# Kernel optimization log

Hardware: AMD Instinct MI355X
Metric: run time of the kernel (lower is better)

The kernel has to match this reference:

```python
import jax, jax.numpy as jnp
from jax import lax
import numpy as np


def _lstm_layer(x, Wih, Whh, bih, bhh):
    # x: [B,T,I]; Wih: [4H,I]; Whh: [4H,H]; gate order i,f,g,o (PyTorch).
    B = x.shape[0]
    H = Whh.shape[1]
    xg = jnp.einsum('bti,gi->btg', x, Wih) + bih + bhh  # [B,T,4H]

    def step(carry, xg_t):
        h, c = carry
        g = xg_t + h @ Whh.T  # [B,4H]
        i, f, gg, o = jnp.split(g, 4, axis=-1)
        i = jax.nn.sigmoid(i)
        f = jax.nn.sigmoid(f)
        gg = jnp.tanh(gg)
        o = jax.nn.sigmoid(o)
        c = f * c + i * gg
        h = o * jnp.tanh(c)
        return (h, c), h

    init = (jnp.zeros((B, H), x.dtype), jnp.zeros((B, H), x.dtype))
    _, hs = lax.scan(step, init, jnp.swapaxes(xg, 0, 1))  # hs: [T,B,H]
    return jnp.swapaxes(hs, 0, 1)  # [B,T,H]


def _uniform(key, shape, k):
    return jax.random.uniform(key, shape, jnp.float32, -k, k)


def setup_inputs() -> dict:
    key = jax.random.key(0)
    ks = jax.random.split(key, 20)
    B, T, D = 64, 512, 2048
    x = jax.random.normal(ks[0], (B, T, D), jnp.float32)
    inp = {'x': x}
    # PyTorch LSTM init: U(-1/sqrt(H), 1/sqrt(H))
    specs = [('1', 2048, 256), ('2', 256, 128), ('3', 128, 64)]
    i = 1
    for tag, I, H in specs:
        k = 1.0 / np.sqrt(H)
        inp['Wih' + tag] = _uniform(ks[i], (4 * H, I), k); i += 1
        inp['Whh' + tag] = _uniform(ks[i], (4 * H, H), k); i += 1
        inp['bih' + tag] = _uniform(ks[i], (4 * H,), k); i += 1
        inp['bhh' + tag] = _uniform(ks[i], (4 * H,), k); i += 1
    kd = 1.0 / np.sqrt(64)
    inp['Wd'] = _uniform(ks[13], (32, 64), kd)
    inp['bd'] = _uniform(ks[14], (32,), kd)
    kw = 1.0 / np.sqrt(2048)
    inp['Ww'] = _uniform(ks[15], (32, 2048), kw)
    inp['bw'] = _uniform(ks[16], (32,), kw)
    ko = 1.0 / np.sqrt(64)
    inp['Wo'] = _uniform(ks[17], (1, 64), ko)
    inp['bo'] = _uniform(ks[18], (1,), ko)
    return inp


def reference(x, Wih1, Whh1, bih1, bhh1, Wih2, Whh2, bih2, bhh2,
              Wih3, Whh3, bih3, bhh3, Wd, bd, Ww, bw, Wo, bo):
    out = _lstm_layer(x, Wih1, Whh1, bih1, bhh1)   # [B,T,256]
    out = _lstm_layer(out, Wih2, Whh2, bih2, bhh2)  # [B,T,128]
    out = _lstm_layer(out, Wih3, Whh3, bih3, bhh3)  # [B,T,64]
    deep = out[:, -1, :]                            # dropout is identity at eval
    deep = jax.nn.relu(deep @ Wd.T + bd)            # [B,32]
    wide = x[:, -1, :]
    wide = jax.nn.relu(wide @ Ww.T + bw)            # [B,32]
    comb = jnp.concatenate([deep, wide], axis=1)    # [B,64]
    return comb @ Wo.T + bo                         # [B,1]
```

## Files before the change

### kernel.cpp

```cpp
#include <hip/hip_runtime.h>

typedef _Float16 f16;
typedef _Float16 f16x2 __attribute__((ext_vector_type(2)));
typedef _Float16 f16x8 __attribute__((ext_vector_type(8)));
typedef float    f32x4 __attribute__((ext_vector_type(4)));

__device__ __forceinline__ f16x2 as_h2(unsigned int u) {
  union { unsigned int u; f16x2 h; } c; c.u = u; return c.h;
}
__device__ __forceinline__ unsigned int pack2(float x, float y) {
  union { f16x2 h; unsigned int u; } c; c.h = f16x2{(f16)x, (f16)y}; return c.u;
}
__device__ __forceinline__ float dot2f(unsigned int w, unsigned int h, float acc) {
#if __has_builtin(__builtin_amdgcn_fdot2)
  return __builtin_amdgcn_fdot2(as_h2(w), as_h2(h), acc, false);
#else
  f16x2 a = as_h2(w), b = as_h2(h);
  return acc + (float)a.x * (float)b.x + (float)a.y * (float)b.y;
#endif
}
__device__ __forceinline__ float sigmoidf_(float x) { return 1.f / (1.f + __expf(-x)); }
__device__ __forceinline__ float tanhf_(float x) { float e = __expf(2.f * x); return 1.f - 2.f / (e + 1.f); }

#define GLDS(gsrc, ldst) __builtin_amdgcn_global_load_lds( \
    (const __attribute__((address_space(1))) void*)(gsrc), \
    (__attribute__((address_space(3))) void*)(ldst), 16, 0, 0)

__global__ void cvt_f32_f16(const float* __restrict__ in, f16* __restrict__ out, long n) {
  long i = ((long)blockIdx.x * blockDim.x + threadIdx.x) * 8;
  long stride = (long)gridDim.x * blockDim.x * 8;
  for (; i < n; i += stride) {
    float4 a = *(const float4*)(in + i);
    float4 b = *(const float4*)(in + i + 4);
    f16x8 h = {(f16)a.x, (f16)a.y, (f16)a.z, (f16)a.w,
               (f16)b.x, (f16)b.y, (f16)b.z, (f16)b.w};
    *(f16x8*)(out + i) = h;
  }
}

template<int K>
__global__ __launch_bounds__(256) void gemm_bias(const f16* __restrict__ A,
                                                 const f16* __restrict__ W,
                                                 const float* __restrict__ bias1,
                                                 const float* __restrict__ bias2,
                                                 float* __restrict__ out, int N) {
  constexpr int BK = 32;
  __shared__ f16 As[2][128 * BK];
  __shared__ f16 Bs[2][128 * BK];
  const int tid = threadIdx.x;
  const int wid = tid >> 6, lane = tid & 63;
  const int m0 = blockIdx.x * 128, n0 = blockIdx.y * 128;
  const int wr = (wid >> 1) * 64, wc = (wid & 1) * 64;
  const int r = lane & 15, kg = lane >> 4;

  f32x4 acc[4][4];
  #pragma unroll
  for (int i = 0; i < 4; ++i)
    #pragma unroll
    for (int j = 0; j < 4; ++j) acc[i][j] = f32x4{0.f, 0.f, 0.f, 0.f};

  auto stage = [&](int buf, int k0) {
    #pragma unroll
    for (int i = 0; i < 2; ++i) {
      int c = tid + 256 * i;
      const f16* asrc = A + (long)(m0 + (c >> 2)) * K + k0 + (c & 3) * 8;
      GLDS(asrc, &As[buf][(64 * wid + 256 * i) * 8]);
      const f16* wsrc = W + (long)(n0 + (c >> 2)) * K + k0 + (c & 3) * 8;
      GLDS(wsrc, &Bs[buf][(64 * wid + 256 * i) * 8]);
    }
  };

  stage(0, 0);
  for (int kt = 0; kt < K / BK; ++kt) {
    __syncthreads();
    if (kt + 1 < K / BK) stage((kt + 1) & 1, (kt + 1) * BK);
    const f16* Ab = As[kt & 1];
    const f16* Bb = Bs[kt & 1];
    f16x8 af[4], bf[4];
    #pragma unroll
    for (int f = 0; f < 4; ++f) {
      af[f] = *(const f16x8*)&Ab[(wr + f * 16 + r) * BK + kg * 8];
      bf[f] = *(const f16x8*)&Bb[(wc + f * 16 + r) * BK + kg * 8];
    }
    #pragma unroll
    for (int mf = 0; mf < 4; ++mf)
      #pragma unroll
      for (int nf = 0; nf < 4; ++nf)
        acc[mf][nf] = __builtin_amdgcn_mfma_f32_16x16x32_f16(af[mf], bf[nf], acc[mf][nf], 0, 0, 0);
  }

  #pragma unroll
  for (int nf = 0; nf < 4; ++nf) {
    int n = n0 + wc + nf * 16 + r;
    float bsum = bias1[n] + bias2[n];
    #pragma unroll
    for (int mf = 0; mf < 4; ++mf) {
      #pragma unroll
      for (int q = 0; q < 4; ++q) {
        int m = m0 + wr + mf * 16 + kg * 4 + q;
        out[(long)m * N + n] = acc[mf][nf][q] + bsum;
      }
    }
  }
}

__global__ __launch_bounds__(512) void lstm_l1(const float* __restrict__ xg,
                                               const float* __restrict__ Whh,
                                               f16* __restrict__ hout) {
  __shared__ uint2 wtail[16][1024];
  __shared__ uint4 hbuf[32];
  __shared__ float gact[1024];
  const int b = blockIdx.x;
  const int t = threadIdx.x;
  const int g0 = t, g1 = t + 512;

  unsigned int w0[96], w1[96];
  #pragma unroll
  for (int p = 0; p < 96; ++p) {
    float2 f0 = *(const float2*)&Whh[g0 * 256 + 2 * p];
    float2 f1 = *(const float2*)&Whh[g1 * 256 + 2 * p];
    w0[p] = pack2(f0.x, f0.y);
    w1[p] = pack2(f1.x, f1.y);
  }
  #pragma unroll
  for (int u = 0; u < 16; ++u) {
    float4 f0 = *(const float4*)&Whh[g0 * 256 + 192 + 4 * u];
    wtail[u][g0] = make_uint2(pack2(f0.x, f0.y), pack2(f0.z, f0.w));
    float4 f1 = *(const float4*)&Whh[g1 * 256 + 192 + 4 * u];
    wtail[u][g1] = make_uint2(pack2(f1.x, f1.y), pack2(f1.z, f1.w));
  }
  if (t < 32) hbuf[t] = make_uint4(0, 0, 0, 0);
  float c = 0.f;
  __syncthreads();

  const bool g1_sig = (t >= 256);
  for (int ts = 0; ts < 512; ++ts) {
    const long base = ((long)b * 512 + ts);
    float a0 = xg[base * 1024 + g0];
    float a1 = xg[base * 1024 + g1];
    #pragma unroll
    for (int i = 0; i < 24; ++i) {
      uint4 hv = hbuf[i];
      a0 = dot2f(w0[4 * i + 0], hv.x, a0); a0 = dot2f(w0[4 * i + 1], hv.y, a0);
      a0 = dot2f(w0[4 * i + 2], hv.z, a0); a0 = dot2f(w0[4 * i + 3], hv.w, a0);
      a1 = dot2f(w1[4 * i + 0], hv.x, a1); a1 = dot2f(w1[4 * i + 1], hv.y, a1);
      a1 = dot2f(w1[4 * i + 2], hv.z, a1); a1 = dot2f(w1[4 * i + 3], hv.w, a1);
    }
    #pragma unroll
    for (int i = 0; i < 8; ++i) {
      uint4 hv = hbuf[24 + i];
      uint2 wa0 = wtail[2 * i][g0], wb0 = wtail[2 * i + 1][g0];
      uint2 wa1 = wtail[2 * i][g1], wb1 = wtail[2 * i + 1][g1];
      a0 = dot2f(wa0.x, hv.x, a0); a0 = dot2f(wa0.y, hv.y, a0);
      a0 = dot2f(wb0.x, hv.z, a0); a0 = dot2f(wb0.y, hv.w, a0);
      a1 = dot2f(wa1.x, hv.x, a1); a1 = dot2f(wa1.y, hv.y, a1);
      a1 = dot2f(wb1.x, hv.z, a1); a1 = dot2f(wb1.y, hv.w, a1);
    }
    gact[g0] = sigmoidf_(a0);
    gact[g1] = g1_sig ? sigmoidf_(a1) : tanhf_(a1);
    __syncthreads();
    if (t < 256) {
      float i_ = gact[t], f_ = gact[256 + t], gg = gact[512 + t], o_ = gact[768 + t];
      c = f_ * c + i_ * gg;
      float hn = o_ * tanhf_(c);
      reinterpret_cast<f16*>(hbuf)[t] = (f16)hn;
      hout[base * 256 + t] = (f16)hn;
    }
    __syncthreads();
  }
}

__global__ __launch_bounds__(512) void lstm_l2(const float* __restrict__ xg,
                                               const float* __restrict__ Whh,
                                               f16* __restrict__ hout) {
  __shared__ uint2 wlds[32][512];
  __shared__ uint4 hbuf[16];
  __shared__ float gact[512];
  const int b = blockIdx.x, t = threadIdx.x;
  #pragma unroll
  for (int u = 0; u < 32; ++u) {
    float4 f = *(const float4*)&Whh[t * 128 + 4 * u];
    wlds[u][t] = make_uint2(pack2(f.x, f.y), pack2(f.z, f.w));
  }
  if (t < 16) hbuf[t] = make_uint4(0, 0, 0, 0);
  float c = 0.f;
  __syncthreads();
  const int type = t >> 7;
  for (int ts = 0; ts < 512; ++ts) {
    const long base = ((long)b * 512 + ts);
    float a = xg[base * 512 + t];
    #pragma unroll
    for (int i = 0; i < 16; ++i) {
      uint4 hv = hbuf[i];
      uint2 wa = wlds[2 * i][t], wb = wlds[2 * i + 1][t];
      a = dot2f(wa.x, hv.x, a); a = dot2f(wa.y, hv.y, a);
      a = dot2f(wb.x, hv.z, a); a = dot2f(wb.y, hv.w, a);
    }
    gact[t] = (type == 2) ? tanhf_(a) : sigmoidf_(a);
    __syncthreads();
    if (t < 128) {
      float i_ = gact[t], f_ = gact[128 + t], gg = gact[256 + t], o_ = gact[384 + t];
      c = f_ * c + i_ * gg;
      float hn = o_ * tanhf_(c);
      reinterpret_cast<f16*>(hbuf)[t] = (f16)hn;
      hout[base * 128 + t] = (f16)hn;
    }
    __syncthreads();
  }
}

__global__ __launch_bounds__(256) void lstm_l3(const float* __restrict__ xg,
                                               const float* __restrict__ Whh,
                                               float* __restrict__ h3last) {
  __shared__ uint2 wlds[16][256];
  __shared__ uint4 hbuf[8];
  __shared__ float gact[256];
  const int b = blockIdx.x, t = threadIdx.x;
  #pragma unroll
  for (int u = 0; u < 16; ++u) {
    float4 f = *(const float4*)&Whh[t * 64 + 4 * u];
    wlds[u][t] = make_uint2(pack2(f.x, f.y), pack2(f.z, f.w));
  }
  if (t < 8) hbuf[t] = make_uint4(0, 0, 0, 0);
  float c = 0.f;
  __syncthreads();
  const int type = t >> 6;
  for (int ts = 0; ts < 512; ++ts) {
    float a = xg[((long)b * 512 + ts) * 256 + t];
    #pragma unroll
    for (int i = 0; i < 8; ++i) {
      uint4 hv = hbuf[i];
      uint2 wa = wlds[2 * i][t], wb = wlds[2 * i + 1][t];
      a = dot2f(wa.x, hv.x, a); a = dot2f(wa.y, hv.y, a);
      a = dot2f(wb.x, hv.z, a); a = dot2f(wb.y, hv.w, a);
    }
    gact[t] = (type == 2) ? tanhf_(a) : sigmoidf_(a);
    __syncthreads();
    if (t < 64) {
      float i_ = gact[t], f_ = gact[64 + t], gg = gact[128 + t], o_ = gact[192 + t];
      c = f_ * c + i_ * gg;
      float hn = o_ * tanhf_(c);
      reinterpret_cast<f16*>(hbuf)[t] = (f16)hn;
      if (ts == 511) h3last[b * 64 + t] = hn;
    }
    __syncthreads();
  }
}

__global__ __launch_bounds__(256) void head_kernel(const float* __restrict__ x,
                                                   const float* __restrict__ h3last,
                                                   const float* __restrict__ Wd, const float* __restrict__ bd,
                                                   const float* __restrict__ Ww, const float* __restrict__ bw,
                                                   const float* __restrict__ Wo, const float* __restrict__ bo,
                                                   float* __restrict__ outp) {
  __shared__ float part[256];
  __shared__ float comb[64];
  const int b = blockIdx.x, t = threadIdx.x;
  const int o = t & 31, seg = t >> 5;
  const float* xl = x + ((long)b * 512 + 511) * 2048;
  float s = 0.f;
  for (int k = seg * 256; k < seg * 256 + 256; ++k) s += xl[k] * Ww[o * 2048 + k];
  part[t] = s;
  __syncthreads();
  if (t < 32) {
    float w = 0.f;
    #pragma unroll
    for (int q = 0; q < 8; ++q) w += part[t + 32 * q];
    w += bw[t];
    comb[32 + t] = fmaxf(w, 0.f);
    float d = bd[t];
    for (int k = 0; k < 64; ++k) d += h3last[b * 64 + k] * Wd[t * 64 + k];
    comb[t] = fmaxf(d, 0.f);
  }
  __syncthreads();
  if (t == 0) {
    float r = bo[0];
    for (int j = 0; j < 64; ++j) r += comb[j] * Wo[j];
    outp[b] = r;
  }
}

static inline int cvt_blocks(long n) {
  long bl = (n / 8 + 255) / 256;
  return (int)(bl > 4096 ? 4096 : bl);
}

extern "C" void kernel_launch(void* const* d_in, const int* in_sizes, int n_in,
                              void* d_out, int out_size, void* d_ws, size_t ws_size,
                              hipStream_t stream) {
  const float* x    = (const float*)d_in[0];
  const float* Wih1 = (const float*)d_in[1];
  const float* Whh1 = (const float*)d_in[2];
  const float* bih1 = (const float*)d_in[3];
  const float* bhh1 = (const float*)d_in[4];
  const float* Wih2 = (const float*)d_in[5];
  const float* Whh2 = (const float*)d_in[6];
  const float* bih2 = (const float*)d_in[7];
  const float* bhh2 = (const float*)d_in[8];
  const float* Wih3 = (const float*)d_in[9];
  const float* Whh3 = (const float*)d_in[10];
  const float* bih3 = (const float*)d_in[11];
  const float* bhh3 = (const float*)d_in[12];
  const float* Wd   = (const float*)d_in[13];
  const float* bd   = (const float*)d_in[14];
  const float* Ww   = (const float*)d_in[15];
  const float* bw   = (const float*)d_in[16];
  const float* Wo   = (const float*)d_in[17];
  const float* bo   = (const float*)d_in[18];

  char* ws = (char*)d_ws;
  f16*   x_h   = (f16*)(ws + 0);
  float* xg1   = (float*)(ws + 134217728);
  f16*   h1    = (f16*)(ws + 268435456);
  f16*   wih1h = (f16*)(ws + 285212672);
  f16*   wih2h = (f16*)(ws + 289406976);
  f16*   wih3h = (f16*)(ws + 289669120);
  float* h3l   = (float*)(ws + 289734656);
  float* xg2   = (float*)(ws + 0);
  f16*   h2    = (f16*)(ws + 134217728);
  float* xg3   = (float*)(ws + 67108864);

  cvt_f32_f16<<<cvt_blocks(67108864), 256, 0, stream>>>(x, x_h, 67108864L);
  cvt_f32_f16<<<cvt_blocks(2097152), 256, 0, stream>>>(Wih1, wih1h, 2097152L);
  cvt_f32_f16<<<cvt_blocks(131072), 256, 0, stream>>>(Wih2, wih2h, 131072L);
  cvt_f32_f16<<<cvt_blocks(32768), 256, 0, stream>>>(Wih3, wih3h, 32768L);

  gemm_bias<2048><<<dim3(256, 8), 256, 0, stream>>>(x_h, wih1h, bih1, bhh1, xg1, 1024);
  lstm_l1<<<64, 512, 0, stream>>>(xg1, Whh1, h1);
  gemm_bias<256><<<dim3(256, 4), 256, 0, stream>>>(h1, wih2h, bih2, bhh2, xg2, 512);
  lstm_l2<<<64, 512, 0, stream>>>(xg2, Whh2, h2);
  gemm_bias<128><<<dim3(256, 2), 256, 0, stream>>>(h2, wih3h, bih3, bhh3, xg3, 256);
  lstm_l3<<<64, 256, 0, stream>>>(xg3, Whh3, h3l);
  head_kernel<<<64, 256, 0, stream>>>(x, h3l, Wd, bd, Ww, bw, Wo, bo, (float*)d_out);
}
```

Before: 2.724 ms.

## Prefetch next-step gate inputs, split dot accumulators, move small-layer weights to registers

In all three recurrent kernels, the next timestep's precomputed input-gate values are loaded during the current step, so global load latency leaves the serial critical path. The recurrent dot products now alternate between two accumulators, shortening the dependent fdot2 chain. Layers 2 and 3 keep their packed recurrent weights in registers instead of LDS, and layer 1 shifts a few weight columns from registers into LDS and adds a two-waves-per-SIMD launch-bounds hint. The cost is higher register pressure in layers 2 and 3, more LDS reads in layer 1, and possible spills if the compiler cannot meet the occupancy hint.

After: 2.308 ms. 15.3% less time.

```diff
diff --git a/kernel.cpp b/kernel.cpp
--- a/kernel.cpp
+++ b/kernel.cpp
@@ -104,29 +104,29 @@
   }
 }
 
-__global__ __launch_bounds__(512) void lstm_l1(const float* __restrict__ xg,
-                                               const float* __restrict__ Whh,
-                                               f16* __restrict__ hout) {
-  __shared__ uint2 wtail[16][1024];
+__global__ __launch_bounds__(512, 2) void lstm_l1(const float* __restrict__ xg,
+                                                  const float* __restrict__ Whh,
+                                                  f16* __restrict__ hout) {
+  __shared__ uint2 wtail[18][1024];
   __shared__ uint4 hbuf[32];
   __shared__ float gact[1024];
   const int b = blockIdx.x;
   const int t = threadIdx.x;
   const int g0 = t, g1 = t + 512;
 
-  unsigned int w0[96], w1[96];
-  #pragma unroll
-  for (int p = 0; p < 96; ++p) {
+  unsigned int w0[92], w1[92];
+  #pragma unroll
+  for (int p = 0; p < 92; ++p) {
     float2 f0 = *(const float2*)&Whh[g0 * 256 + 2 * p];
     float2 f1 = *(const float2*)&Whh[g1 * 256 + 2 * p];
     w0[p] = pack2(f0.x, f0.y);
     w1[p] = pack2(f1.x, f1.y);
   }
   #pragma unroll
-  for (int u = 0; u < 16; ++u) {
-    float4 f0 = *(const float4*)&Whh[g0 * 256 + 192 + 4 * u];
+  for (int u = 0; u < 18; ++u) {
+    float4 f0 = *(const float4*)&Whh[g0 * 256 + 184 + 4 * u];
     wtail[u][g0] = make_uint2(pack2(f0.x, f0.y), pack2(f0.z, f0.w));
-    float4 f1 = *(const float4*)&Whh[g1 * 256 + 192 + 4 * u];
+    float4 f1 = *(const float4*)&Whh[g1 * 256 + 184 + 4 * u];
     wtail[u][g1] = make_uint2(pack2(f1.x, f1.y), pack2(f1.z, f1.w));
   }
   if (t < 32) hbuf[t] = make_uint4(0, 0, 0, 0);
@@ -134,28 +134,48 @@
   __syncthreads();
 
   const bool g1_sig = (t >= 256);
+  const long rowbase = (long)b * 512;
+  float a0 = xg[rowbase * 1024 + g0];
+  float a1 = xg[rowbase * 1024 + g1];
   for (int ts = 0; ts < 512; ++ts) {
-    const long base = ((long)b * 512 + ts);
-    float a0 = xg[base * 1024 + g0];
-    float a1 = xg[base * 1024 + g1];
-    #pragma unroll
-    for (int i = 0; i < 24; ++i) {
+    const long base = rowbase + ts;
+    const long nb = rowbase + (ts < 511 ? ts + 1 : 511);
+    float a0n = xg[nb * 1024 + g0];
+    float a1n = xg[nb * 1024 + g1];
+    float s0 = 0.f, s1 = 0.f;
+    #pragma unroll
+    for (int i = 0; i < 23; ++i) {
       uint4 hv = hbuf[i];
-      a0 = dot2f(w0[4 * i + 0], hv.x, a0); a0 = dot2f(w0[4 * i + 1], hv.y, a0);
-      a0 = dot2f(w0[4 * i + 2], hv.z, a0); a0 = dot2f(w0[4 * i + 3], hv.w, a0);
-      a1 = dot2f(w1[4 * i + 0], hv.x, a1); a1 = dot2f(w1[4 * i + 1], hv.y, a1);
-      a1 = dot2f(w1[4 * i + 2], hv.z, a1); a1 = dot2f(w1[4 * i + 3], hv.w, a1);
-    }
-    #pragma unroll
-    for (int i = 0; i < 8; ++i) {
-      uint4 hv = hbuf[24 + i];
-      uint2 wa0 = wtail[2 * i][g0], wb0 = wtail[2 * i + 1][g0];
-      uint2 wa1 = wtail[2 * i][g1], wb1 = wtail[2 * i + 1][g1];
-      a0 = dot2f(wa0.x, hv.x, a0); a0 = dot2f(wa0.y, hv.y, a0);
-      a0 = dot2f(wb0.x, hv.z, a0); a0 = dot2f(wb0.y, hv.w, a0);
-      a1 = dot2f(wa1.x, hv.x, a1); a1 = dot2f(wa1.y, hv.y, a1);
-      a1 = dot2f(wb1.x, hv.z, a1); a1 = dot2f(wb1.y, hv.w, a1);
-    }
+      if (i & 1) {
+        s0 = dot2f(w0[4 * i + 0], hv.x, s0); s0 = dot2f(w0[4 * i + 1], hv.y, s0);
+        s0 = dot2f(w0[4 * i + 2], hv.z, s0); s0 = dot2f(w0[4 * i + 3], hv.w, s0);
+        s1 = dot2f(w1[4 * i + 0], hv.x, s1); s1 = dot2f(w1[4 * i + 1], hv.y, s1);
+        s1 = dot2f(w1[4 * i + 2], hv.z, s1); s1 = dot2f(w1[4 * i + 3], hv.w, s1);
+      } else {
+        a0 = dot2f(w0[4 * i + 0], hv.x, a0); a0 = dot2f(w0[4 * i + 1], hv.y, a0);
+        a0 = dot2f(w0[4 * i + 2], hv.z, a0); a0 = dot2f(w0[4 * i + 3], hv.w, a0);
+        a1 = dot2f(w1[4 * i + 0], hv.x, a1); a1 = dot2f(w1[4 * i + 1], hv.y, a1);
+        a1 = dot2f(w1[4 * i + 2], hv.z, a1); a1 = dot2f(w1[4 * i + 3], hv.w, a1);
+      }
+    }
+    #pragma unroll
+    for (int j = 0; j < 9; ++j) {
+      uint4 hv = hbuf[23 + j];
+      uint2 wa0 = wtail[2 * j][g0], wb0 = wtail[2 * j + 1][g0];
+      uint2 wa1 = wtail[2 * j][g1], wb1 = wtail[2 * j + 1][g1];
+      if (j & 1) {
+        s0 = dot2f(wa0.x, hv.x, s0); s0 = dot2f(wa0.y, hv.y, s0);
+        s0 = dot2f(wb0.x, hv.z, s0); s0 = dot2f(wb0.y, hv.w, s0);
+        s1 = dot2f(wa1.x, hv.x, s1); s1 = dot2f(wa1.y, hv.y, s1);
+        s1 = dot2f(wb1.x, hv.z, s1); s1 = dot2f(wb1.y, hv.w, s1);
+      } else {
+        a0 = dot2f(wa0.x, hv.x, a0); a0 = dot2f(wa0.y, hv.y, a0);
+        a0 = dot2f(wb0.x, hv.z, a0); a0 = dot2f(wb0.y, hv.w, a0);
+        a1 = dot2f(wa1.x, hv.x, a1); a1 = dot2f(wa1.y, hv.y, a1);
+        a1 = dot2f(wb1.x, hv.z, a1); a1 = dot2f(wb1.y, hv.w, a1);
+      }
+    }
+    a0 += s0; a1 += s1;
     gact[g0] = sigmoidf_(a0);
     gact[g1] = g1_sig ? sigmoidf_(a1) : tanhf_(a1);
     __syncthreads();
@@ -167,35 +187,45 @@
       hout[base * 256 + t] = (f16)hn;
     }
     __syncthreads();
+    a0 = a0n; a1 = a1n;
   }
 }
 
 __global__ __launch_bounds__(512) void lstm_l2(const float* __restrict__ xg,
                                                const float* __restrict__ Whh,
                                                f16* __restrict__ hout) {
-  __shared__ uint2 wlds[32][512];
   __shared__ uint4 hbuf[16];
   __shared__ float gact[512];
   const int b = blockIdx.x, t = threadIdx.x;
-  #pragma unroll
-  for (int u = 0; u < 32; ++u) {
-    float4 f = *(const float4*)&Whh[t * 128 + 4 * u];
-    wlds[u][t] = make_uint2(pack2(f.x, f.y), pack2(f.z, f.w));
+  unsigned int w[64];
+  #pragma unroll
+  for (int p = 0; p < 64; ++p) {
+    float2 f = *(const float2*)&Whh[t * 128 + 2 * p];
+    w[p] = pack2(f.x, f.y);
   }
   if (t < 16) hbuf[t] = make_uint4(0, 0, 0, 0);
   float c = 0.f;
   __syncthreads();
   const int type = t >> 7;
+  const long rowbase = (long)b * 512;
+  float a = xg[rowbase * 512 + t];
   for (int ts = 0; ts < 512; ++ts) {
-    const long base = ((long)b * 512 + ts);
-    float a = xg[base * 512 + t];
+    const long base = rowbase + ts;
+    const long nb = rowbase + (ts < 511 ? ts + 1 : 511);
+    float an = xg[nb * 512 + t];
+    float s = 0.f;
     #pragma unroll
     for (int i = 0; i < 16; ++i) {
       uint4 hv = hbuf[i];
-      uint2 wa = wlds[2 * i][t], wb = wlds[2 * i + 1][t];
-      a = dot2f(wa.x, hv.x, a); a = dot2f(wa.y, hv.y, a);
-      a = dot2f(wb.x, hv.z, a); a = dot2f(wb.y, hv.w, a);
-    }
+      if (i & 1) {
+        s = dot2f(w[4 * i + 0], hv.x, s); s = dot2f(w[4 * i + 1], hv.y, s);
+        s = dot2f(w[4 * i + 2], hv.z, s); s = dot2f(w[4 * i + 3], hv.w, s);
+      } else {
+        a = dot2f(w[4 * i + 0], hv.x, a); a = dot2f(w[4 * i + 1], hv.y, a);
+        a = dot2f(w[4 * i + 2], hv.z, a); a = dot2f(w[4 * i + 3], hv.w, a);
+      }
+    }
+    a += s;
     gact[t] = (type == 2) ? tanhf_(a) : sigmoidf_(a);
     __syncthreads();
     if (t < 128) {
@@ -206,34 +236,44 @@
       hout[base * 128 + t] = (f16)hn;
     }
     __syncthreads();
+    a = an;
   }
 }
 
 __global__ __launch_bounds__(256) void lstm_l3(const float* __restrict__ xg,
                                                const float* __restrict__ Whh,
                                                float* __restrict__ h3last) {
-  __shared__ uint2 wlds[16][256];
   __shared__ uint4 hbuf[8];
   __shared__ float gact[256];
   const int b = blockIdx.x, t = threadIdx.x;
-  #pragma unroll
-  for (int u = 0; u < 16; ++u) {
-    float4 f = *(const float4*)&Whh[t * 64 + 4 * u];
-    wlds[u][t] = make_uint2(pack2(f.x, f.y), pack2(f.z, f.w));
+  unsigned int w[32];
+  #pragma unroll
+  for (int p = 0; p < 32; ++p) {
+    float2 f = *(const float2*)&Whh[t * 64 + 2 * p];
+    w[p] = pack2(f.x, f.y);
   }
   if (t < 8) hbuf[t] = make_uint4(0, 0, 0, 0);
   float c = 0.f;
   __syncthreads();
   const int type = t >> 6;
+  const long rowbase = (long)b * 512;
+  float a = xg[rowbase * 256 + t];
   for (int ts = 0; ts < 512; ++ts) {
-    float a = xg[((long)b * 512 + ts) * 256 + t];
+    const long nb = rowbase + (ts < 511 ? ts + 1 : 511);
+    float an = xg[nb * 256 + t];
+    float s = 0.f;
     #pragma unroll
     for (int i = 0; i < 8; ++i) {
       uint4 hv = hbuf[i];
-      uint2 wa = wlds[2 * i][t], wb = wlds[2 * i + 1][t];
-      a = dot2f(wa.x, hv.x, a); a = dot2f(wa.y, hv.y, a);
-      a = dot2f(wb.x, hv.z, a); a = dot2f(wb.y, hv.w, a);
-    }
+      if (i & 1) {
+        s = dot2f(w[4 * i + 0], hv.x, s); s = dot2f(w[4 * i + 1], hv.y, s);
+        s = dot2f(w[4 * i + 2], hv.z, s); s = dot2f(w[4 * i + 3], hv.w, s);
+      } else {
+        a = dot2f(w[4 * i + 0], hv.x, a); a = dot2f(w[4 * i + 1], hv.y, a);
+        a = dot2f(w[4 * i + 2], hv.z, a); a = dot2f(w[4 * i + 3], hv.w, a);
+      }
+    }
+    a += s;
     gact[t] = (type == 2) ? tanhf_(a) : sigmoidf_(a);
     __syncthreads();
     if (t < 64) {
@@ -244,6 +284,7 @@
       if (ts == 511) h3last[b * 64 + t] = hn;
     }
     __syncthreads();
+    a = an;
   }
 }
 
```
